# Optimization experiments

Hardware: AMD Instinct MI355X
Metric: run time of the kernel (lower is better)

## Reference

```python
import jax, jax.numpy as jnp
import numpy as np

N_I = 500_000   # 'indivi' nodes (dst)
N_H = 200_000   # 'house' nodes
F_I = 32        # indivi feature dim
F_H = 16        # house feature dim
EF = 8          # edge_attr dim
E1 = 2_000_000  # house->indivi edges
E2 = 2_000_000  # indivi->indivi edges


def setup_inputs() -> dict:
    key = jax.random.key(0)
    ks = jax.random.split(key, 16)
    return {
        "x_indivi": jax.random.normal(ks[0], (N_I, F_I), jnp.float32),
        "x_house": jax.random.normal(ks[1], (N_H, F_H), jnp.float32),
        "edge_attr_h2i": jax.random.normal(ks[2], (E1, EF), jnp.float32),
        "edge_attr_i2i": jax.random.normal(ks[3], (E2, EF), jnp.float32),
        "W_edge_h2i": jax.random.normal(ks[4], (F_H, EF), jnp.float32) * 0.1,
        "b_edge_h2i": jax.random.normal(ks[5], (F_H,), jnp.float32) * 0.1,
        "W_edge_i2i": jax.random.normal(ks[6], (F_I, EF), jnp.float32) * 0.1,
        "b_edge_i2i": jax.random.normal(ks[7], (F_I,), jnp.float32) * 0.1,
        "W_root_h2i": jax.random.normal(ks[8], (1, F_I), jnp.float32) * 0.1,
        "bias_h2i": jax.random.normal(ks[9], (1,), jnp.float32) * 0.1,
        "W_root_i2i": jax.random.normal(ks[10], (1, F_I), jnp.float32) * 0.1,
        "bias_i2i": jax.random.normal(ks[11], (1,), jnp.float32) * 0.1,
        "src_h2i": jax.random.randint(ks[12], (E1,), 0, N_H, jnp.int32),
        "dst_h2i": jax.random.randint(ks[13], (E1,), 0, N_I, jnp.int32),
        "src_i2i": jax.random.randint(ks[14], (E2,), 0, N_I, jnp.int32),
        "dst_i2i": jax.random.randint(ks[15], (E2,), 0, N_I, jnp.int32),
    }


def _nnconv(x_src, x_dst, edge_attr, src, dst, W_edge, b_edge, W_root, bias, num_dst):
    # Edge MLP -> per-edge weight matrix of shape [F_src, out=1], flattened to [E, F_src]
    w = edge_attr @ W_edge.T + b_edge                     # [E, F_src]
    # message_e = x_src[src_e] @ w_e  (out_channels = 1)
    msg = jnp.sum(x_src[src] * w, axis=-1, keepdims=True)  # [E, 1]
    agg = jax.ops.segment_sum(msg, dst, num_segments=num_dst)  # [N_dst, 1]
    # root transform on destination features + bias
    return agg + x_dst @ W_root.T + bias                  # [N_dst, 1]


def reference(x_indivi, x_house, edge_attr_h2i, edge_attr_i2i,
              W_edge_h2i, b_edge_h2i, W_edge_i2i, b_edge_i2i,
              W_root_h2i, bias_h2i, W_root_i2i, bias_i2i,
              src_h2i, dst_h2i, src_i2i, dst_i2i):
    out_h = _nnconv(x_house, x_indivi, edge_attr_h2i, src_h2i, dst_h2i,
                    W_edge_h2i, b_edge_h2i, W_root_h2i, bias_h2i, N_I)
    out_i = _nnconv(x_indivi, x_indivi, edge_attr_i2i, src_i2i, dst_i2i,
                    W_edge_i2i, b_edge_i2i, W_root_i2i, bias_i2i, N_I)
    # HeteroConv(aggr='sum') over the two relations targeting 'indivi'
    return out_h + out_i
```

## Files before the change

kernel.cpp:

```cpp
#include <hip/hip_runtime.h>
#include <hip/hip_bf16.h>

#define N_I 500000
#define N_H 200000
#define E1  2000000
#define E2  2000000

template<int F, bool ROOT>
__global__ __launch_bounds__(256) void precompute_g(
    const float* __restrict__ x, const float* __restrict__ W, const float* __restrict__ b,
    float* __restrict__ g, int n,
    const float* __restrict__ rW1, const float* __restrict__ rW2,
    const float* __restrict__ rb1, const float* __restrict__ rb2,
    float* __restrict__ out)
{
    __shared__ float Wf[F * 8];
    __shared__ float bv[F];
    __shared__ float wr[F];

    for (int i = threadIdx.x; i < F * 8; i += 256) Wf[i] = W[i];
    if (threadIdx.x < F) {
        bv[threadIdx.x] = b[threadIdx.x];
        if (ROOT) wr[threadIdx.x] = rW1[threadIdx.x] + rW2[threadIdx.x];
    }
    __syncthreads();

    int nid = blockIdx.x * 256 + threadIdx.x;
    if (nid >= n) return;

    float xv[F];
    const float4* xp = (const float4*)(x + (size_t)nid * F);
    #pragma unroll
    for (int q = 0; q < F / 4; q++) {
        float4 v = xp[q];
        xv[q*4+0] = v.x; xv[q*4+1] = v.y; xv[q*4+2] = v.z; xv[q*4+3] = v.w;
    }

    float acc[9];
    #pragma unroll
    for (int k = 0; k < 9; k++) acc[k] = 0.f;

    #pragma unroll
    for (int j = 0; j < F; j++) {
        float4 w0 = *(const float4*)(Wf + j * 8);
        float4 w1 = *(const float4*)(Wf + j * 8 + 4);
        float xj = xv[j];
        acc[0] = fmaf(xj, w0.x, acc[0]);
        acc[1] = fmaf(xj, w0.y, acc[1]);
        acc[2] = fmaf(xj, w0.z, acc[2]);
        acc[3] = fmaf(xj, w0.w, acc[3]);
        acc[4] = fmaf(xj, w1.x, acc[4]);
        acc[5] = fmaf(xj, w1.y, acc[5]);
        acc[6] = fmaf(xj, w1.z, acc[6]);
        acc[7] = fmaf(xj, w1.w, acc[7]);
        acc[8] = fmaf(xj, bv[j], acc[8]);
    }

    float4* gp = (float4*)(g + (size_t)nid * 12);
    gp[0] = make_float4(acc[0], acc[1], acc[2], acc[3]);
    gp[1] = make_float4(acc[4], acc[5], acc[6], acc[7]);
    gp[2] = make_float4(acc[8], 0.f, 0.f, 0.f);

    if (ROOT) {
        float r = rb1[0] + rb2[0];
        #pragma unroll
        for (int j = 0; j < F; j++) r = fmaf(xv[j], wr[j], r);
        out[nid] = r;
    }
}

__global__ __launch_bounds__(256) void edge_kernel(
    const int* __restrict__ src1, const int* __restrict__ dst1,
    const float* __restrict__ ea1, const float* __restrict__ g1,
    const int* __restrict__ src2, const int* __restrict__ dst2,
    const float* __restrict__ ea2, const float* __restrict__ g2,
    float* __restrict__ out)
{
    int t = blockIdx.x * 256 + threadIdx.x;
    if (t >= E1 + E2) return;
    const int* srcp; const int* dstp; const float* eap; const float* gp;
    int e;
    if (t < E1) { e = t;      srcp = src1; dstp = dst1; eap = ea1; gp = g1; }
    else        { e = t - E1; srcp = src2; dstp = dst2; eap = ea2; gp = g2; }

    int s = srcp[e];
    int d = dstp[e];
    const float4* ap = (const float4*)(eap + (size_t)e * 8);
    float4 a0 = ap[0];
    float4 a1 = ap[1];
    const float4* gr = (const float4*)(gp + (size_t)s * 12);
    float4 ga = gr[0];
    float4 gb = gr[1];
    float4 gc = gr[2];

    float msg = gc.x;
    msg = fmaf(a0.x, ga.x, msg);
    msg = fmaf(a0.y, ga.y, msg);
    msg = fmaf(a0.z, ga.z, msg);
    msg = fmaf(a0.w, ga.w, msg);
    msg = fmaf(a1.x, gb.x, msg);
    msg = fmaf(a1.y, gb.y, msg);
    msg = fmaf(a1.z, gb.z, msg);
    msg = fmaf(a1.w, gb.w, msg);

    atomicAdd(out + d, msg);
}

extern "C" void kernel_launch(void* const* d_in, const int* in_sizes, int n_in,
                              void* d_out, int out_size, void* d_ws, size_t ws_size,
                              hipStream_t stream) {
    const float* x_i  = (const float*)d_in[0];
    const float* x_h  = (const float*)d_in[1];
    const float* ea_h = (const float*)d_in[2];
    const float* ea_i = (const float*)d_in[3];
    const float* We_h = (const float*)d_in[4];
    const float* be_h = (const float*)d_in[5];
    const float* We_i = (const float*)d_in[6];
    const float* be_i = (const float*)d_in[7];
    const float* Wr_h = (const float*)d_in[8];
    const float* br_h = (const float*)d_in[9];
    const float* Wr_i = (const float*)d_in[10];
    const float* br_i = (const float*)d_in[11];
    const int* src_h = (const int*)d_in[12];
    const int* dst_h = (const int*)d_in[13];
    const int* src_i = (const int*)d_in[14];
    const int* dst_i = (const int*)d_in[15];

    float* out = (float*)d_out;

    char* ws = (char*)d_ws;
    float* g_i = (float*)ws;
    float* g_h = (float*)(ws + 24000000);

    precompute_g<16, false><<<(N_H + 255) / 256, 256, 0, stream>>>(
        x_h, We_h, be_h, g_h, N_H, nullptr, nullptr, nullptr, nullptr, nullptr);
    precompute_g<32, true><<<(N_I + 255) / 256, 256, 0, stream>>>(
        x_i, We_i, be_i, g_i, N_I, Wr_h, Wr_i, br_h, br_i, out);
    edge_kernel<<<(E1 + E2 + 255) / 256, 256, 0, stream>>>(
        src_h, dst_h, ea_h, g_h, src_i, dst_i, ea_i, g_i, out);
}
```

Baseline: 407.0 us.

## Replace global scatter atomics with bucketed counting-sort and shared-memory reduction

```diff
diff --git a/kernel.cpp b/kernel.cpp
--- a/kernel.cpp
+++ b/kernel.cpp
@@ -1,10 +1,17 @@
 #include <hip/hip_runtime.h>
-#include <hip/hip_bf16.h>
 
 #define N_I 500000
 #define N_H 200000
 #define E1  2000000
 #define E2  2000000
+#define TOTAL_E (E1 + E2)
+
+#define NB 512
+#define CHUNK 8192
+#define NWG ((TOTAL_E + CHUNK - 1) / CHUNK)
+#define NB_RED ((N_I + 1023) / 1024)
+
+static_assert(NWG <= 512, "scan assumes <=512 workgroups");
 
 template<int F, bool ROOT>
 __global__ __launch_bounds__(256) void precompute_g(
@@ -69,22 +76,21 @@
     }
 }
 
-__global__ __launch_bounds__(256) void edge_kernel(
+__device__ __forceinline__ void edge_msg(
+    int t,
     const int* __restrict__ src1, const int* __restrict__ dst1,
     const float* __restrict__ ea1, const float* __restrict__ g1,
     const int* __restrict__ src2, const int* __restrict__ dst2,
     const float* __restrict__ ea2, const float* __restrict__ g2,
-    float* __restrict__ out)
-{
-    int t = blockIdx.x * 256 + threadIdx.x;
-    if (t >= E1 + E2) return;
+    int& d_out, float& m_out)
+{
     const int* srcp; const int* dstp; const float* eap; const float* gp;
     int e;
     if (t < E1) { e = t;      srcp = src1; dstp = dst1; eap = ea1; gp = g1; }
     else        { e = t - E1; srcp = src2; dstp = dst2; eap = ea2; gp = g2; }
 
     int s = srcp[e];
-    int d = dstp[e];
+    d_out = dstp[e];
     const float4* ap = (const float4*)(eap + (size_t)e * 8);
     float4 a0 = ap[0];
     float4 a1 = ap[1];
@@ -102,8 +108,130 @@
     msg = fmaf(a1.y, gb.y, msg);
     msg = fmaf(a1.z, gb.z, msg);
     msg = fmaf(a1.w, gb.w, msg);
-
-    atomicAdd(out + d, msg);
+    m_out = msg;
+}
+
+__global__ __launch_bounds__(256) void msg_hist_kernel(
+    const int* __restrict__ src1, const int* __restrict__ dst1,
+    const float* __restrict__ ea1, const float* __restrict__ g1,
+    const int* __restrict__ src2, const int* __restrict__ dst2,
+    const float* __restrict__ ea2, const float* __restrict__ g2,
+    float* __restrict__ msg_out, int* __restrict__ H)
+{
+    __shared__ int hist[NB];
+    for (int i = threadIdx.x; i < NB; i += 256) hist[i] = 0;
+    __syncthreads();
+
+    int base = blockIdx.x * CHUNK;
+    #pragma unroll 2
+    for (int it = 0; it < CHUNK / 256; ++it) {
+        int t = base + it * 256 + threadIdx.x;
+        if (t < TOTAL_E) {
+            int d; float m;
+            edge_msg(t, src1, dst1, ea1, g1, src2, dst2, ea2, g2, d, m);
+            msg_out[t] = m;
+            atomicAdd(&hist[d >> 10], 1);
+        }
+    }
+    __syncthreads();
+    for (int i = threadIdx.x; i < NB; i += 256) H[blockIdx.x * NB + i] = hist[i];
+}
+
+__global__ __launch_bounds__(512) void scan_cols_kernel(int* __restrict__ H,
+                                                        int* __restrict__ total)
+{
+    __shared__ int v[512];
+    int b = blockIdx.x;
+    int tid = threadIdx.x;
+    int orig = (tid < NWG) ? H[tid * NB + b] : 0;
+    v[tid] = orig;
+    __syncthreads();
+    for (int off = 1; off < 512; off <<= 1) {
+        int t = (tid >= off) ? v[tid - off] : 0;
+        __syncthreads();
+        v[tid] += t;
+        __syncthreads();
+    }
+    if (tid < NWG) H[tid * NB + b] = v[tid] - orig;
+    if (tid == 511) total[b] = v[511];
+}
+
+__global__ __launch_bounds__(512) void scan_base_kernel(const int* __restrict__ total,
+                                                        int* __restrict__ base)
+{
+    __shared__ int v[512];
+    int tid = threadIdx.x;
+    int orig = total[tid];
+    v[tid] = orig;
+    __syncthreads();
+    for (int off = 1; off < 512; off <<= 1) {
+        int t = (tid >= off) ? v[tid - off] : 0;
+        __syncthreads();
+        v[tid] += t;
+        __syncthreads();
+    }
+    base[tid] = v[tid] - orig;
+}
+
+__global__ __launch_bounds__(256) void scatter_kernel(
+    const int* __restrict__ dst1, const int* __restrict__ dst2,
+    const float* __restrict__ msg, const int* __restrict__ H,
+    const int* __restrict__ base, uint2* __restrict__ pairs)
+{
+    __shared__ int cur[NB];
+    for (int i = threadIdx.x; i < NB; i += 256)
+        cur[i] = H[blockIdx.x * NB + i] + base[i];
+    __syncthreads();
+
+    int cbase = blockIdx.x * CHUNK;
+    #pragma unroll 2
+    for (int it = 0; it < CHUNK / 256; ++it) {
+        int t = cbase + it * 256 + threadIdx.x;
+        if (t < TOTAL_E) {
+            int d = (t < E1) ? dst1[t] : dst2[t - E1];
+            float m = msg[t];
+            int pos = atomicAdd(&cur[d >> 10], 1);
+            pairs[pos] = make_uint2((unsigned)d, __float_as_uint(m));
+        }
+    }
+}
+
+__global__ __launch_bounds__(256) void reduce_kernel(
+    const uint2* __restrict__ pairs, const int* __restrict__ base,
+    const int* __restrict__ total, float* __restrict__ out)
+{
+    __shared__ float acc[1024];
+    for (int i = threadIdx.x; i < 1024; i += 256) acc[i] = 0.f;
+    __syncthreads();
+
+    int b = blockIdx.x;
+    int start = base[b];
+    int cnt = total[b];
+    for (int i = threadIdx.x; i < cnt; i += 256) {
+        uint2 p = pairs[start + i];
+        atomicAdd(&acc[p.x & 1023], __uint_as_float(p.y));
+    }
+    __syncthreads();
+
+    int nb = b << 10;
+    for (int i = threadIdx.x; i < 1024; i += 256) {
+        int n = nb + i;
+        if (n < N_I) out[n] += acc[i];
+    }
+}
+
+__global__ __launch_bounds__(256) void edge_kernel_atomic(
+    const int* __restrict__ src1, const int* __restrict__ dst1,
+    const float* __restrict__ ea1, const float* __restrict__ g1,
+    const int* __restrict__ src2, const int* __restrict__ dst2,
+    const float* __restrict__ ea2, const float* __restrict__ g2,
+    float* __restrict__ out)
+{
+    int t = blockIdx.x * 256 + threadIdx.x;
+    if (t >= TOTAL_E) return;
+    int d; float m;
+    edge_msg(t, src1, dst1, ea1, g1, src2, dst2, ea2, g2, d, m);
+    atomicAdd(out + d, m);
 }
 
 extern "C" void kernel_launch(void* const* d_in, const int* in_sizes, int n_in,
@@ -131,11 +259,28 @@
     char* ws = (char*)d_ws;
     float* g_i = (float*)ws;
     float* g_h = (float*)(ws + 24000000);
+    float* msg = (float*)(ws + 33600000);
+    int*   H   = (int*)  (ws + 49600000);
+    int*   tot = (int*)  (ws + 50603008);
+    int*   bas = (int*)  (ws + 50605056);
+    uint2* pairs = (uint2*)ws;
+    const size_t WS_NEEDED = 50607104;
 
     precompute_g<16, false><<<(N_H + 255) / 256, 256, 0, stream>>>(
         x_h, We_h, be_h, g_h, N_H, nullptr, nullptr, nullptr, nullptr, nullptr);
     precompute_g<32, true><<<(N_I + 255) / 256, 256, 0, stream>>>(
         x_i, We_i, be_i, g_i, N_I, Wr_h, Wr_i, br_h, br_i, out);
-    edge_kernel<<<(E1 + E2 + 255) / 256, 256, 0, stream>>>(
-        src_h, dst_h, ea_h, g_h, src_i, dst_i, ea_i, g_i, out);
-}
+
+    if (ws_size >= WS_NEEDED) {
+        msg_hist_kernel<<<NWG, 256, 0, stream>>>(
+            src_h, dst_h, ea_h, g_h, src_i, dst_i, ea_i, g_i, msg, H);
+        scan_cols_kernel<<<NB, 512, 0, stream>>>(H, tot);
+        scan_base_kernel<<<1, 512, 0, stream>>>(tot, bas);
+        scatter_kernel<<<NWG, 256, 0, stream>>>(
+            dst_h, dst_i, msg, H, bas, pairs);
+        reduce_kernel<<<NB_RED, 256, 0, stream>>>(pairs, bas, tot, out);
+    } else {
+        edge_kernel_atomic<<<(TOTAL_E + 255) / 256, 256, 0, stream>>>(
+            src_h, dst_h, ea_h, g_h, src_i, dst_i, ea_i, g_i, out);
+    }
+}
```

Result: faster. 384.9 us (-5.4%).
